# Optimization experiments

Hardware: AMD Instinct MI355X
Metric: run time of the kernel (lower is better)

The kernel has to match this reference:

```python
import jax, jax.numpy as jnp
import numpy as np

B, C, H, W = 4, 256, 64, 64
CI = 128  # inter_channels = in_channels // 2
EPS = 1e-5  # torch BatchNorm default eps


def setup_inputs() -> dict:
    key = jax.random.key(0)
    ks = jax.random.split(key, 8)

    def w(k, shape, s=0.02):
        return jax.random.normal(k, shape, jnp.float32) * s

    return {
        "x": jax.random.normal(ks[0], (B, C, H, W), jnp.float32),
        # theta (Q) linear + BatchNorm1d (inference-mode running stats)
        "theta_w": w(ks[1], (CI, C)), "theta_b": jnp.zeros((CI,), jnp.float32),
        "theta_bn_gamma": jnp.ones((CI,), jnp.float32), "theta_bn_beta": jnp.zeros((CI,), jnp.float32),
        "theta_bn_mean": jnp.zeros((CI,), jnp.float32), "theta_bn_var": jnp.ones((CI,), jnp.float32),
        # phi (K) linear + BatchNorm1d
        "phi_w": w(ks[2], (CI, C)), "phi_b": jnp.zeros((CI,), jnp.float32),
        "phi_bn_gamma": jnp.ones((CI,), jnp.float32), "phi_bn_beta": jnp.zeros((CI,), jnp.float32),
        "phi_bn_mean": jnp.zeros((CI,), jnp.float32), "phi_bn_var": jnp.ones((CI,), jnp.float32),
        # g (V) linear
        "g_w": w(ks[3], (CI, C)), "g_b": jnp.zeros((CI,), jnp.float32),
        # W_z output linear
        "wz_w": w(ks[4], (C, CI)), "wz_b": jnp.zeros((C,), jnp.float32),
        # output BatchNorm2d (gamma nonzero instead of init-0 so output is non-trivial)
        "bn_gamma": w(ks[5], (C,), 0.1), "bn_beta": jnp.zeros((C,), jnp.float32),
        "bn_mean": jnp.zeros((C,), jnp.float32), "bn_var": jnp.ones((C,), jnp.float32),
    }


def _linear(z, w, b):
    # z: [B, N, C], w: [D, C] -> [B, N, D]
    return jnp.einsum('bnc,dc->bnd', z, w) + b


def _bn(z, gamma, beta, mean, var):
    # per-channel affine BN in inference mode, channel on last axis
    return (z - mean) * jax.lax.rsqrt(var + EPS) * gamma + beta


def reference(x, theta_w, theta_b, theta_bn_gamma, theta_bn_beta, theta_bn_mean, theta_bn_var,
              phi_w, phi_b, phi_bn_gamma, phi_bn_beta, phi_bn_mean, phi_bn_var,
              g_w, g_b, wz_w, wz_b, bn_gamma, bn_beta, bn_mean, bn_var):
    b, c, h, w = x.shape
    n = h * w
    ci = theta_w.shape[0]
    scale = float(ci) ** (-0.5)

    x_flat = x.reshape(b, c, n).transpose(0, 2, 1)  # [B, N, C]
    Q = _bn(_linear(x_flat, theta_w, theta_b), theta_bn_gamma, theta_bn_beta, theta_bn_mean, theta_bn_var)
    K = _bn(_linear(x_flat, phi_w, phi_b), phi_bn_gamma, phi_bn_beta, phi_bn_mean, phi_bn_var)
    V = _linear(x_flat, g_w, g_b)  # [B, N, CI]

    # attention computed in fp32 (matches torch amp-disabled block)
    attn = jnp.einsum('bnd,bmd->bnm', Q.astype(jnp.float32), K.astype(jnp.float32)) * scale
    attn = jax.nn.softmax(attn, axis=-1).astype(V.dtype)  # [B, N, N]

    y = jnp.einsum('bnm,bmd->bnd', attn, V)  # [B, N, CI]
    y = jnp.einsum('bnd,cd->bnc', y, wz_w) + wz_b  # [B, N, C]
    y = y.transpose(0, 2, 1).reshape(b, c, h, w)

    # BatchNorm2d (inference mode), channel axis 1
    rstd = jax.lax.rsqrt(bn_var + EPS)
    y = (y - bn_mean[None, :, None, None]) * (rstd * bn_gamma)[None, :, None, None] + bn_beta[None, :, None, None]
    return y + x
```

## Files before the change

kernel.cpp:

```cpp
#include <hip/hip_runtime.h>
#include <stdint.h>

typedef __attribute__((ext_vector_type(8))) short bf16x8;
typedef __attribute__((ext_vector_type(4))) float f32x4;

#define WS_WQKV   0u
#define WS_WZ     196608u
#define WS_SCL    262144u
#define WS_SHF    263680u
#define WS_WZS    265216u
#define WS_WZT    266240u
#define WS_Q      524288u
#define WS_K      (WS_Q  + 4194304u)
#define WS_VT     (WS_K  + 4194304u)
#define WS_Y      (WS_VT + 4194304u)
#define WS_OP     (WS_Y  + 4194304u)
#define WS_LP     (WS_OP + 16777216u)

__device__ __forceinline__ short f2bf(float f) {
  union { float f; uint32_t u; } v; v.f = f;
  uint32_t r = v.u + 0x7fffu + ((v.u >> 16) & 1u);
  return (short)(r >> 16);
}

__device__ __forceinline__ uint32_t pack2_bf16(float a, float b) {
  union { float f; uint32_t u; } x, y; x.f = a; y.f = b;
  return ((y.u + 0x8000u) & 0xffff0000u) | ((x.u + 0x8000u) >> 16);
}

__device__ __forceinline__ f32x4 mfma16(bf16x8 a, bf16x8 b, f32x4 c) {
  return __builtin_amdgcn_mfma_f32_16x16x32_bf16(a, b, c, 0, 0, 0);
}

__device__ __forceinline__ void load_lds16(const short* gp, short* lp) {
  __builtin_amdgcn_global_load_lds(
      (const __attribute__((address_space(1))) uint32_t*)gp,
      (__attribute__((address_space(3))) uint32_t*)lp, 16, 0, 0);
}

__global__ __launch_bounds__(256) void prep_kernel(
    const float* theta_w, const float* phi_w, const float* g_w, const float* wz_w,
    const float* theta_b, const float* tg, const float* tb, const float* tm, const float* tv,
    const float* phi_b,   const float* pg, const float* pb, const float* pm, const float* pv,
    const float* g_b,
    const float* wz_b, const float* bg, const float* bb, const float* bm, const float* bv,
    char* ws) {
  int idx = blockIdx.x * 256 + threadIdx.x;
  short* wqkv = (short*)(ws + WS_WQKV);
  if (idx < 98304) {
    float w;
    if (idx < 32768) w = theta_w[idx];
    else if (idx < 65536) w = phi_w[idx - 32768];
    else w = g_w[idx - 65536];
    wqkv[idx] = f2bf(w);
  }
  if (idx < 32768) ((short*)(ws + WS_WZ))[idx] = f2bf(wz_w[idx]);
  if (idx < 384) {
    float s, t;
    if (idx < 128)      { s = tg[idx] * rsqrtf(tv[idx] + 1e-5f);
                          t = (theta_b[idx] - tm[idx]) * s + tb[idx]; }
    else if (idx < 256) { int d = idx - 128; s = pg[d] * rsqrtf(pv[d] + 1e-5f);
                          t = (phi_b[d] - pm[d]) * s + pb[d]; }
    else                { int d = idx - 256; s = 1.0f; t = g_b[d]; }
    ((float*)(ws + WS_SCL))[idx] = s;
    ((float*)(ws + WS_SHF))[idx] = t;
  }
  if (idx < 256) {
    float s = bg[idx] * rsqrtf(bv[idx] + 1e-5f);
    float t = (wz_b[idx] - bm[idx]) * s + bb[idx];
    ((float*)(ws + WS_WZS))[idx] = s;
    ((float*)(ws + WS_WZT))[idx] = t;
  }
}

__global__ __launch_bounds__(256) void qkv_kernel(const float* __restrict__ x, char* ws) {
  const int nt2 = blockIdx.x, b = blockIdx.y;
  const int t = threadIdx.x;
  __shared__ __attribute__((aligned(16))) short xs[32][264];
  const short* wqkv = (const short*)(ws + WS_WQKV);
  const float* scl = (const float*)(ws + WS_SCL);
  const float* shf = (const float*)(ws + WS_SHF);
  const int n0 = nt2 * 32;
  #pragma unroll
  for (int i = 0; i < 8; ++i) {
    int chunk = i * 256 + t;
    int c = chunk >> 3, n4 = chunk & 7;
    const float4 v = *(const float4*)(x + ((size_t)(b * 256 + c) << 12) + n0 + n4 * 4);
    xs[n4 * 4 + 0][c] = f2bf(v.x);
    xs[n4 * 4 + 1][c] = f2bf(v.y);
    xs[n4 * 4 + 2][c] = f2bf(v.z);
    xs[n4 * 4 + 3][c] = f2bf(v.w);
  }
  __syncthreads();
  const int wv = t >> 6, l = t & 63, lr = l & 15, q = l >> 4;
  const int wn = wv & 1, dh = wv >> 1;
  bf16x8 a[8];
  #pragma unroll
  for (int kt = 0; kt < 8; ++kt) a[kt] = *(const bf16x8*)&xs[wn * 16 + lr][kt * 32 + q * 8];
  f32x4 acc[12] = {};
  #pragma unroll
  for (int kt = 0; kt < 8; ++kt) {
    #pragma unroll
    for (int s = 0; s < 12; ++s) {
      const short* wp = wqkv + (size_t)(dh * 192 + s * 16 + lr) * 256 + kt * 32 + q * 8;
      bf16x8 bf = *(const bf16x8*)wp;
      acc[s] = mfma16(a[kt], bf, acc[s]);
    }
  }
  const float s2 = 0.08838834764831845f * 1.4426950408889634f;
  #pragma unroll
  for (int s = 0; s < 12; ++s) {
    int dg = dh * 192 + s * 16 + lr;
    float sc = scl[dg], sh = shf[dg];
    if (dg < 128) { sc *= s2; sh *= s2; }
    short vals[4];
    #pragma unroll
    for (int r = 0; r < 4; ++r) vals[r] = f2bf(acc[s][r] * sc + sh);
    int nbase = n0 + wn * 16 + q * 4;
    if (dg < 128) {
      short* Q = (short*)(ws + WS_Q) + ((size_t)b << 19);
      #pragma unroll
      for (int r = 0; r < 4; ++r) Q[(size_t)(nbase + r) * 128 + dg] = vals[r];
    } else if (dg < 256) {
      int d = dg - 128;
      short* Kt = (short*)(ws + WS_K) + ((size_t)b << 19);
      int kt2 = d >> 5, qa = (d >> 3) & 3, e = d & 7;
      int tile = nbase >> 6, sg = (nbase >> 4) & 3, lr0 = nbase & 15;
      size_t base = ((size_t)((tile * 16 + sg * 4 + kt2) * 64 + qa * 16 + lr0) << 3) + e;
      #pragma unroll
      for (int r = 0; r < 4; ++r) Kt[base + r * 8] = vals[r];
    } else {
      int d = dg - 256;
      short* Vt = (short*)(ws + WS_VT) + ((size_t)b << 19);
      int dt = d >> 4, lrv = d & 15;
      int tile = nbase >> 6, mm = nbase & 63;
      int h = mm >> 5, qv = (mm >> 3) & 3, e0 = mm & 7;
      size_t base = ((size_t)((tile * 16 + dt * 2 + h) * 64 + qv * 16 + lrv) << 3) + e0;
      short4 pk; pk.x = vals[0]; pk.y = vals[1]; pk.z = vals[2]; pk.w = vals[3];
      *(short4*)(Vt + base) = pk;
    }
  }
}

__global__ __launch_bounds__(256, 2) void attn_kernel(char* ws) {
  const int g = blockIdx.x;
  const int b = (g & 7) >> 1;
  const int idx = ((g >> 3) << 1) | (g & 1);
  const int nt = idx >> 2, mc = idx & 3;
  const int t = threadIdx.x, w = t >> 6, l = t & 63, lr = l & 15, q = l >> 4;
  __shared__ __attribute__((aligned(16))) short ks0[16][512];
  __shared__ __attribute__((aligned(16))) short vs0[16][512];
  __shared__ __attribute__((aligned(16))) short ks1[16][512];
  __shared__ __attribute__((aligned(16))) short vs1[16][512];
  __shared__ __attribute__((aligned(16))) short psl[4][2][2][512];
  const short* Q  = (const short*)(ws + WS_Q)  + ((size_t)b << 19);
  const short* Kt = (const short*)(ws + WS_K)  + ((size_t)b << 19);
  const short* Vt = (const short*)(ws + WS_VT) + ((size_t)b << 19);
  const int n0w = nt * 128 + w * 32;
  bf16x8 qf[2][4];
  #pragma unroll
  for (int j = 0; j < 2; ++j) {
    const short* qp = Q + (size_t)(n0w + j * 16 + lr) * 128 + q * 8;
    #pragma unroll
    for (int kt = 0; kt < 4; ++kt) qf[j][kt] = *(const bf16x8*)(qp + kt * 32);
  }
  f32x4 o[2][8] = {};
  float lsum[2] = {0.f, 0.f};

  const short* kbase = Kt + (size_t)(mc * 16) * 8192;
  const short* vbase = Vt + (size_t)(mc * 16) * 8192;

  auto stage = [&](short (*KS)[512], short (*VS)[512], int it) {
    const short* kg = kbase + (size_t)it * 8192;
    const short* vg = vbase + (size_t)it * 8192;
    #pragma unroll
    for (int i = 0; i < 4; ++i) {
      int gi = i * 4 + w;
      load_lds16(kg + gi * 512 + l * 8, &KS[gi][0]);
      load_lds16(vg + gi * 512 + l * 8, &VS[gi][0]);
    }
  };

  auto compute = [&](short (*ksl)[512], short (*vsl)[512]) {
    f32x4 sacc[2][4] = {};
    __builtin_amdgcn_s_setprio(1);
    #pragma unroll
    for (int kt = 0; kt < 4; ++kt) {
      #pragma unroll
      for (int s = 0; s < 4; ++s) {
        bf16x8 kf = *(const bf16x8*)&ksl[s * 4 + kt][l * 8];
        sacc[0][s] = mfma16(kf, qf[0][kt], sacc[0][s]);
        sacc[1][s] = mfma16(kf, qf[1][kt], sacc[1][s]);
      }
    }
    __builtin_amdgcn_s_setprio(0);
    #pragma unroll
    for (int j = 0; j < 2; ++j) {
      #pragma unroll
      for (int s = 0; s < 4; ++s) {
        float e0 = exp2f(sacc[j][s][0]);
        float e1 = exp2f(sacc[j][s][1]);
        float e2 = exp2f(sacc[j][s][2]);
        float e3 = exp2f(sacc[j][s][3]);
        lsum[j] += (e0 + e1) + (e2 + e3);
        uint2 pk;
        pk.x = pack2_bf16(e0, e1);
        pk.y = pack2_bf16(e2, e3);
        *(uint2*)&psl[w][j][s >> 1][(((s & 1) * 2 + (q >> 1)) * 16 + lr) * 8 + (q & 1) * 4] = pk;
      }
    }
    bf16x8 pf[2][2];
    #pragma unroll
    for (int j = 0; j < 2; ++j)
      #pragma unroll
      for (int h = 0; h < 2; ++h)
        pf[j][h] = *(const bf16x8*)&psl[w][j][h][l * 8];
    __builtin_amdgcn_s_setprio(1);
    #pragma unroll
    for (int dt = 0; dt < 8; ++dt) {
      #pragma unroll
      for (int h = 0; h < 2; ++h) {
        bf16x8 vf = *(const bf16x8*)&vsl[dt * 2 + h][l * 8];
        o[0][dt] = mfma16(vf, pf[0][h], o[0][dt]);
        o[1][dt] = mfma16(vf, pf[1][h], o[1][dt]);
      }
    }
    __builtin_amdgcn_s_setprio(0);
  };

  stage(ks0, vs0, 0);
  __syncthreads();
  for (int it2 = 0; it2 < 8; ++it2) {
    stage(ks1, vs1, it2 * 2 + 1);
    compute(ks0, vs0);
    __syncthreads();
    if (it2 < 7) stage(ks0, vs0, it2 * 2 + 2);
    compute(ks1, vs1);
    __syncthreads();
  }

  const int cb = mc * 4 + b;
  float* LP = (float*)(ws + WS_LP) + ((size_t)cb << 12);
  #pragma unroll
  for (int j = 0; j < 2; ++j) {
    float s = lsum[j];
    s += __shfl_xor(s, 16, 64);
    s += __shfl_xor(s, 32, 64);
    if (l < 16) LP[n0w + j * 16 + l] = s;
  }
  short* OPc = (short*)(ws + WS_OP) + ((size_t)cb << 19);
  #pragma unroll
  for (int j = 0; j < 2; ++j)
    #pragma unroll
    for (int dt = 0; dt < 8; ++dt) {
      short4 pk;
      pk.x = f2bf(o[j][dt][0]); pk.y = f2bf(o[j][dt][1]);
      pk.z = f2bf(o[j][dt][2]); pk.w = f2bf(o[j][dt][3]);
      *(short4*)&OPc[((size_t)(n0w + j * 16 + lr) << 7) + dt * 16 + q * 4] = pk;
    }
}

__global__ __launch_bounds__(256) void proj_kernel(const float* __restrict__ x,
                                                   char* ws, float* __restrict__ out) {
  const int nt = blockIdx.x, b = blockIdx.y;
  const int t = threadIdx.x, wv = t >> 6, l = t & 63, lr = l & 15, q = l >> 4;
  __shared__ __attribute__((aligned(16))) short ys[16][136];
  const short* OP = (const short*)(ws + WS_OP);
  const float* LP = (const float*)(ws + WS_LP);
  const short* WZ = (const short*)(ws + WS_WZ);
  const float* wzs = (const float*)(ws + WS_WZS);
  const float* wzt = (const float*)(ws + WS_WZT);
  const int n0 = nt * 16;
  {
    int row = t >> 4, d8 = (t & 15) * 8;
    int n = n0 + row;
    float acc8[8] = {};
    float lsf = 0.f;
    #pragma unroll
    for (int mc = 0; mc < 4; ++mc) {
      int cb = mc * 4 + b;
      const short* p = OP + ((size_t)cb << 19) + ((size_t)n << 7) + d8;
      uint4 v = *(const uint4*)p;
      uint32_t uu[4] = {v.x, v.y, v.z, v.w};
      #pragma unroll
      for (int w = 0; w < 4; ++w) {
        union { uint32_t u; float f; } lo, hi;
        lo.u = uu[w] << 16; hi.u = uu[w] & 0xffff0000u;
        acc8[w * 2 + 0] += lo.f;
        acc8[w * 2 + 1] += hi.f;
      }
      lsf += LP[(cb << 12) + n];
    }
    float inv = 1.0f / lsf;
    short out8[8];
    #pragma unroll
    for (int j = 0; j < 8; ++j) out8[j] = f2bf(acc8[j] * inv);
    *(uint4*)&ys[row][d8] = *(uint4*)out8;
  }
  __syncthreads();
  bf16x8 a[4];
  #pragma unroll
  for (int kt = 0; kt < 4; ++kt) a[kt] = *(const bf16x8*)&ys[lr][kt * 32 + q * 8];
  f32x4 acc[4] = {};
  #pragma unroll
  for (int kt = 0; kt < 4; ++kt) {
    #pragma unroll
    for (int s = 0; s < 4; ++s) {
      const short* wp = WZ + (size_t)(wv * 64 + s * 16 + lr) * 128 + kt * 32 + q * 8;
      bf16x8 bf = *(const bf16x8*)wp;
      acc[s] = mfma16(a[kt], bf, acc[s]);
    }
  }
  #pragma unroll
  for (int s = 0; s < 4; ++s) {
    int c = wv * 64 + s * 16 + lr;
    float sc = wzs[c], sh = wzt[c];
    int nbase = n0 + q * 4;
    size_t base = ((size_t)(b * 256 + c) << 12) + nbase;
    float4 xv = *(const float4*)(x + base);
    float4 ov;
    ov.x = acc[s][0] * sc + sh + xv.x;
    ov.y = acc[s][1] * sc + sh + xv.y;
    ov.z = acc[s][2] * sc + sh + xv.z;
    ov.w = acc[s][3] * sc + sh + xv.w;
    *(float4*)(out + base) = ov;
  }
}

extern "C" void kernel_launch(void* const* d_in, const int* in_sizes, int n_in,
                              void* d_out, int out_size, void* d_ws, size_t ws_size,
                              hipStream_t stream) {
  const float* x       = (const float*)d_in[0];
  const float* theta_w = (const float*)d_in[1];
  const float* theta_b = (const float*)d_in[2];
  const float* tg      = (const float*)d_in[3];
  const float* tb      = (const float*)d_in[4];
  const float* tm      = (const float*)d_in[5];
  const float* tv      = (const float*)d_in[6];
  const float* phi_w   = (const float*)d_in[7];
  const float* phi_b   = (const float*)d_in[8];
  const float* pg      = (const float*)d_in[9];
  const float* pb      = (const float*)d_in[10];
  const float* pm      = (const float*)d_in[11];
  const float* pv      = (const float*)d_in[12];
  const float* g_w     = (const float*)d_in[13];
  const float* g_b     = (const float*)d_in[14];
  const float* wz_w    = (const float*)d_in[15];
  const float* wz_b    = (const float*)d_in[16];
  const float* bg      = (const float*)d_in[17];
  const float* bb      = (const float*)d_in[18];
  const float* bm      = (const float*)d_in[19];
  const float* bv      = (const float*)d_in[20];
  char* ws = (char*)d_ws;
  float* out = (float*)d_out;

  prep_kernel<<<384, 256, 0, stream>>>(theta_w, phi_w, g_w, wz_w,
                                       theta_b, tg, tb, tm, tv,
                                       phi_b, pg, pb, pm, pv,
                                       g_b, wz_b, bg, bb, bm, bv, ws);
  qkv_kernel<<<dim3(128, 4), 256, 0, stream>>>(x, ws);
  attn_kernel<<<512, 256, 0, stream>>>(ws);
  proj_kernel<<<dim3(256, 4), 256, 0, stream>>>(x, ws, out);
}
```

Measured before the change: 200.0 us.

## Switch attention to 32x32x16 MFMA with permlane32 swap instead of LDS P round-trip

Result: no change. 197.1 us (-1.5%).

```diff
diff --git a/kernel.cpp b/kernel.cpp
--- a/kernel.cpp
+++ b/kernel.cpp
@@ -3,6 +3,8 @@
 
 typedef __attribute__((ext_vector_type(8))) short bf16x8;
 typedef __attribute__((ext_vector_type(4))) float f32x4;
+typedef __attribute__((ext_vector_type(16))) float f32x16;
+typedef __attribute__((ext_vector_type(2))) unsigned int uint2v;
 
 #define WS_WQKV   0u
 #define WS_WZ     196608u
@@ -30,6 +32,9 @@
 
 __device__ __forceinline__ f32x4 mfma16(bf16x8 a, bf16x8 b, f32x4 c) {
   return __builtin_amdgcn_mfma_f32_16x16x32_bf16(a, b, c, 0, 0, 0);
+}
+__device__ __forceinline__ f32x16 mfma32(bf16x8 a, bf16x8 b, f32x16 c) {
+  return __builtin_amdgcn_mfma_f32_32x32x16_bf16(a, b, c, 0, 0, 0);
 }
 
 __device__ __forceinline__ void load_lds16(const short* gp, short* lp) {
@@ -76,15 +81,15 @@
 __global__ __launch_bounds__(256) void qkv_kernel(const float* __restrict__ x, char* ws) {
   const int nt2 = blockIdx.x, b = blockIdx.y;
   const int t = threadIdx.x;
-  __shared__ __attribute__((aligned(16))) short xs[32][264];
+  __shared__ __attribute__((aligned(16))) short xs[16][264];
   const short* wqkv = (const short*)(ws + WS_WQKV);
   const float* scl = (const float*)(ws + WS_SCL);
   const float* shf = (const float*)(ws + WS_SHF);
-  const int n0 = nt2 * 32;
-  #pragma unroll
-  for (int i = 0; i < 8; ++i) {
+  const int n0 = nt2 * 16;
+  #pragma unroll
+  for (int i = 0; i < 4; ++i) {
     int chunk = i * 256 + t;
-    int c = chunk >> 3, n4 = chunk & 7;
+    int c = chunk >> 2, n4 = chunk & 3;
     const float4 v = *(const float4*)(x + ((size_t)(b * 256 + c) << 12) + n0 + n4 * 4);
     xs[n4 * 4 + 0][c] = f2bf(v.x);
     xs[n4 * 4 + 1][c] = f2bf(v.y);
@@ -93,30 +98,30 @@
   }
   __syncthreads();
   const int wv = t >> 6, l = t & 63, lr = l & 15, q = l >> 4;
-  const int wn = wv & 1, dh = wv >> 1;
   bf16x8 a[8];
   #pragma unroll
-  for (int kt = 0; kt < 8; ++kt) a[kt] = *(const bf16x8*)&xs[wn * 16 + lr][kt * 32 + q * 8];
-  f32x4 acc[12] = {};
+  for (int kt = 0; kt < 8; ++kt) a[kt] = *(const bf16x8*)&xs[lr][kt * 32 + q * 8];
+  f32x4 acc[6] = {};
   #pragma unroll
   for (int kt = 0; kt < 8; ++kt) {
     #pragma unroll
-    for (int s = 0; s < 12; ++s) {
-      const short* wp = wqkv + (size_t)(dh * 192 + s * 16 + lr) * 256 + kt * 32 + q * 8;
+    for (int s = 0; s < 6; ++s) {
+      const short* wp = wqkv + (size_t)(wv * 96 + s * 16 + lr) * 256 + kt * 32 + q * 8;
       bf16x8 bf = *(const bf16x8*)wp;
       acc[s] = mfma16(a[kt], bf, acc[s]);
     }
   }
   const float s2 = 0.08838834764831845f * 1.4426950408889634f;
   #pragma unroll
-  for (int s = 0; s < 12; ++s) {
-    int dg = dh * 192 + s * 16 + lr;
+  for (int s = 0; s < 6; ++s) {
+    int dg = wv * 96 + s * 16 + lr;
     float sc = scl[dg], sh = shf[dg];
     if (dg < 128) { sc *= s2; sh *= s2; }
     short vals[4];
     #pragma unroll
     for (int r = 0; r < 4; ++r) vals[r] = f2bf(acc[s][r] * sc + sh);
-    int nbase = n0 + wn * 16 + q * 4;
+    int nbase = n0 + q * 4;
+    int tile = nbase >> 6, nn = nbase & 63;
     if (dg < 128) {
       short* Q = (short*)(ws + WS_Q) + ((size_t)b << 19);
       #pragma unroll
@@ -124,18 +129,19 @@
     } else if (dg < 256) {
       int d = dg - 128;
       short* Kt = (short*)(ws + WS_K) + ((size_t)b << 19);
-      int kt2 = d >> 5, qa = (d >> 3) & 3, e = d & 7;
-      int tile = nbase >> 6, sg = (nbase >> 4) & 3, lr0 = nbase & 15;
-      size_t base = ((size_t)((tile * 16 + sg * 4 + kt2) * 64 + qa * 16 + lr0) << 3) + e;
+      int ks = d >> 4, h = (d >> 3) & 1, e = d & 7;
+      int mb = nn >> 5, rr = nn & 31;
+      size_t base = (size_t)tile * 8192 + (size_t)(mb * 8 + ks) * 512
+                  + (size_t)(h * 32 + rr) * 8 + e;
       #pragma unroll
       for (int r = 0; r < 4; ++r) Kt[base + r * 8] = vals[r];
     } else {
       int d = dg - 256;
       short* Vt = (short*)(ws + WS_VT) + ((size_t)b << 19);
-      int dt = d >> 4, lrv = d & 15;
-      int tile = nbase >> 6, mm = nbase & 63;
-      int h = mm >> 5, qv = (mm >> 3) & 3, e0 = mm & 7;
-      size_t base = ((size_t)((tile * 16 + dt * 2 + h) * 64 + qv * 16 + lrv) << 3) + e0;
+      int dt = d >> 5, rv = d & 31;
+      int ks2 = nn >> 4, hv = (nn >> 3) & 1, e0 = nn & 7;
+      size_t base = (size_t)tile * 8192 + (size_t)(dt * 4 + ks2) * 512
+                  + (size_t)(hv * 32 + rv) * 8 + e0;
       short4 pk; pk.x = vals[0]; pk.y = vals[1]; pk.z = vals[2]; pk.w = vals[3];
       *(short4*)(Vt + base) = pk;
     }
@@ -147,25 +153,22 @@
   const int b = (g & 7) >> 1;
   const int idx = ((g >> 3) << 1) | (g & 1);
   const int nt = idx >> 2, mc = idx & 3;
-  const int t = threadIdx.x, w = t >> 6, l = t & 63, lr = l & 15, q = l >> 4;
+  const int t = threadIdx.x, w = t >> 6, l = t & 63;
+  const int lq = l & 31, h = l >> 5;
   __shared__ __attribute__((aligned(16))) short ks0[16][512];
   __shared__ __attribute__((aligned(16))) short vs0[16][512];
   __shared__ __attribute__((aligned(16))) short ks1[16][512];
   __shared__ __attribute__((aligned(16))) short vs1[16][512];
-  __shared__ __attribute__((aligned(16))) short psl[4][2][2][512];
   const short* Q  = (const short*)(ws + WS_Q)  + ((size_t)b << 19);
   const short* Kt = (const short*)(ws + WS_K)  + ((size_t)b << 19);
   const short* Vt = (const short*)(ws + WS_VT) + ((size_t)b << 19);
   const int n0w = nt * 128 + w * 32;
-  bf16x8 qf[2][4];
-  #pragma unroll
-  for (int j = 0; j < 2; ++j) {
-    const short* qp = Q + (size_t)(n0w + j * 16 + lr) * 128 + q * 8;
-    #pragma unroll
-    for (int kt = 0; kt < 4; ++kt) qf[j][kt] = *(const bf16x8*)(qp + kt * 32);
-  }
-  f32x4 o[2][8] = {};
-  float lsum[2] = {0.f, 0.f};
+  bf16x8 qf[8];
+  #pragma unroll
+  for (int ks = 0; ks < 8; ++ks)
+    qf[ks] = *(const bf16x8*)(Q + (size_t)(n0w + lq) * 128 + ks * 16 + h * 8);
+  f32x16 o[4] = {};
+  float lsum = 0.f;
 
   const short* kbase = Kt + (size_t)(mc * 16) * 8192;
   const short* vbase = Vt + (size_t)(mc * 16) * 8192;
@@ -182,47 +185,46 @@
   };
 
   auto compute = [&](short (*ksl)[512], short (*vsl)[512]) {
-    f32x4 sacc[2][4] = {};
+    f32x16 sacc[2] = {};
     __builtin_amdgcn_s_setprio(1);
     #pragma unroll
-    for (int kt = 0; kt < 4; ++kt) {
-      #pragma unroll
-      for (int s = 0; s < 4; ++s) {
-        bf16x8 kf = *(const bf16x8*)&ksl[s * 4 + kt][l * 8];
-        sacc[0][s] = mfma16(kf, qf[0][kt], sacc[0][s]);
-        sacc[1][s] = mfma16(kf, qf[1][kt], sacc[1][s]);
+    for (int ks = 0; ks < 8; ++ks) {
+      #pragma unroll
+      for (int mb = 0; mb < 2; ++mb) {
+        bf16x8 kf = *(const bf16x8*)&ksl[mb * 8 + ks][l * 8];
+        sacc[mb] = mfma32(kf, qf[ks], sacc[mb]);
       }
     }
     __builtin_amdgcn_s_setprio(0);
-    #pragma unroll
-    for (int j = 0; j < 2; ++j) {
-      #pragma unroll
-      for (int s = 0; s < 4; ++s) {
-        float e0 = exp2f(sacc[j][s][0]);
-        float e1 = exp2f(sacc[j][s][1]);
-        float e2 = exp2f(sacc[j][s][2]);
-        float e3 = exp2f(sacc[j][s][3]);
-        lsum[j] += (e0 + e1) + (e2 + e3);
-        uint2 pk;
-        pk.x = pack2_bf16(e0, e1);
-        pk.y = pack2_bf16(e2, e3);
-        *(uint2*)&psl[w][j][s >> 1][(((s & 1) * 2 + (q >> 1)) * 16 + lr) * 8 + (q & 1) * 4] = pk;
-      }
-    }
-    bf16x8 pf[2][2];
-    #pragma unroll
-    for (int j = 0; j < 2; ++j)
-      #pragma unroll
-      for (int h = 0; h < 2; ++h)
-        pf[j][h] = *(const bf16x8*)&psl[w][j][h][l * 8];
+    bf16x8 pf[4];
+    #pragma unroll
+    for (int mb = 0; mb < 2; ++mb) {
+      float e[16];
+      #pragma unroll
+      for (int r = 0; r < 16; ++r) {
+        e[r] = exp2f(sacc[mb][r]);
+        lsum += e[r];
+      }
+      #pragma unroll
+      for (int k = 0; k < 2; ++k) {
+        uint32_t va0 = pack2_bf16(e[8 * k + 0], e[8 * k + 1]);
+        uint32_t va1 = pack2_bf16(e[8 * k + 2], e[8 * k + 3]);
+        uint32_t vb0 = pack2_bf16(e[8 * k + 4], e[8 * k + 5]);
+        uint32_t vb1 = pack2_bf16(e[8 * k + 6], e[8 * k + 7]);
+        uint2v s0 = __builtin_amdgcn_permlane32_swap(va0, vb0, false, false);
+        uint2v s1 = __builtin_amdgcn_permlane32_swap(va1, vb1, false, false);
+        union { uint32_t u[4]; bf16x8 v; } pk;
+        pk.u[0] = s0[0]; pk.u[1] = s1[0]; pk.u[2] = s0[1]; pk.u[3] = s1[1];
+        pf[2 * mb + k] = pk.v;
+      }
+    }
     __builtin_amdgcn_s_setprio(1);
     #pragma unroll
-    for (int dt = 0; dt < 8; ++dt) {
-      #pragma unroll
-      for (int h = 0; h < 2; ++h) {
-        bf16x8 vf = *(const bf16x8*)&vsl[dt * 2 + h][l * 8];
-        o[0][dt] = mfma16(vf, pf[0][h], o[0][dt]);
-        o[1][dt] = mfma16(vf, pf[1][h], o[1][dt]);
+    for (int dt = 0; dt < 4; ++dt) {
+      #pragma unroll
+      for (int ks2 = 0; ks2 < 4; ++ks2) {
+        bf16x8 vf = *(const bf16x8*)&vsl[dt * 4 + ks2][l * 8];
+        o[dt] = mfma32(vf, pf[ks2], o[dt]);
       }
     }
     __builtin_amdgcn_s_setprio(0);
@@ -241,23 +243,24 @@
 
   const int cb = mc * 4 + b;
   float* LP = (float*)(ws + WS_LP) + ((size_t)cb << 12);
-  #pragma unroll
-  for (int j = 0; j < 2; ++j) {
-    float s = lsum[j];
-    s += __shfl_xor(s, 16, 64);
+  {
+    float s = lsum;
     s += __shfl_xor(s, 32, 64);
-    if (l < 16) LP[n0w + j * 16 + l] = s;
+    if (l < 32) LP[n0w + l] = s;
   }
   short* OPc = (short*)(ws + WS_OP) + ((size_t)cb << 19);
   #pragma unroll
-  for (int j = 0; j < 2; ++j)
-    #pragma unroll
-    for (int dt = 0; dt < 8; ++dt) {
+  for (int dt = 0; dt < 4; ++dt) {
+    #pragma unroll
+    for (int rg = 0; rg < 4; ++rg) {
       short4 pk;
-      pk.x = f2bf(o[j][dt][0]); pk.y = f2bf(o[j][dt][1]);
-      pk.z = f2bf(o[j][dt][2]); pk.w = f2bf(o[j][dt][3]);
-      *(short4*)&OPc[((size_t)(n0w + j * 16 + lr) << 7) + dt * 16 + q * 4] = pk;
-    }
+      pk.x = f2bf(o[dt][rg * 4 + 0]);
+      pk.y = f2bf(o[dt][rg * 4 + 1]);
+      pk.z = f2bf(o[dt][rg * 4 + 2]);
+      pk.w = f2bf(o[dt][rg * 4 + 3]);
+      *(short4*)&OPc[((size_t)(n0w + lq) << 7) + dt * 32 + rg * 8 + h * 4] = pk;
+    }
+  }
 }
 
 __global__ __launch_bounds__(256) void proj_kernel(const float* __restrict__ x,
@@ -358,7 +361,7 @@
                                        theta_b, tg, tb, tm, tv,
                                        phi_b, pg, pb, pm, pv,
                                        g_b, wz_b, bg, bb, bm, bv, ws);
-  qkv_kernel<<<dim3(128, 4), 256, 0, stream>>>(x, ws);
+  qkv_kernel<<<dim3(256, 4), 256, 0, stream>>>(x, ws);
   attn_kernel<<<512, 256, 0, stream>>>(ws);
   proj_kernel<<<dim3(256, 4), 256, 0, stream>>>(x, ws, out);
 }
```
